# Performance work log

Hardware: AMD Instinct MI355X
Metric: run time of the kernel (lower is better)

The kernel has to match this reference:

```python
import jax, jax.numpy as jnp
import numpy as np

B, L, D = 2, 1024, 512          # batch, seq_len, d_model
H, DK, DV, P = 8, 64, 64, 4     # heads, d_k, d_v, num masks
TEMP = DK ** 0.5
EPS = 1e-6


def setup_inputs() -> dict:
    key = jax.random.key(0)
    ks = jax.random.split(key, 11)
    s = 0.04  # ~xavier scale for these fan sizes
    q = jax.random.normal(ks[0], (B, L, D), jnp.float32)
    k = jax.random.normal(ks[1], (B, L, D), jnp.float32)
    v = jax.random.normal(ks[2], (B, L, D), jnp.float32)
    mask = (jax.random.uniform(ks[3], (P, 1, 1, L, L)) > 0.2).astype(jnp.float32)
    w_q = jax.random.normal(ks[4], (H * DK, D), jnp.float32) * s
    w_k = jax.random.normal(ks[5], (H * DK, D), jnp.float32) * s
    w_v = jax.random.normal(ks[6], (H * DV, D), jnp.float32) * s
    fc_w = jax.random.normal(ks[7], (D, H * DV), jnp.float32) * s
    fc_b = jnp.zeros((D,), jnp.float32)
    ln_g = jnp.ones((D,), jnp.float32)
    ln_b = jnp.zeros((D,), jnp.float32)
    return {"q": q, "k": k, "v": v, "mask": mask, "w_q": w_q, "w_k": w_k,
            "w_v": w_v, "fc_w": fc_w, "fc_b": fc_b, "ln_g": ln_g, "ln_b": ln_b}


def reference(q, k, v, mask, w_q, w_k, w_v, fc_w, fc_b, ln_g, ln_b):
    b, lq = q.shape[0], q.shape[1]
    lk = k.shape[1]
    residual = q
    # pre-LayerNorm on q (normalize_before=True)
    mu = jnp.mean(q, axis=-1, keepdims=True)
    var = jnp.mean(jnp.square(q - mu), axis=-1, keepdims=True)
    qn = (q - mu) * jax.lax.rsqrt(var + EPS) * ln_g + ln_b
    # projections -> [B,H,L,dk/dv]
    qh = jnp.einsum('bld,ed->ble', qn, w_q).reshape(b, lq, H, DK).transpose(0, 2, 1, 3)
    kh = jnp.einsum('bld,ed->ble', k, w_k).reshape(b, lk, H, DK).transpose(0, 2, 1, 3)
    vh = jnp.einsum('bld,ed->ble', v, w_v).reshape(b, lk, H, DV).transpose(0, 2, 1, 3)
    # shared scores, computed once: [B,H,Lq,Lk]
    attn = jnp.einsum('bhqd,bhkd->bhqk', qh / TEMP, kh)
    # per-mask additive bias, vectorized over P (dropout is identity in eval)
    ext = (1.0 - mask) * -10000.0                      # [P,1,1,Lq,Lk]
    probs = jax.nn.softmax(attn[None] + ext, axis=-1)  # [P,B,H,Lq,Lk]
    out = jnp.einsum('pbhqk,bhkd->pbhqd', probs, vh)   # [P,B,H,Lq,DV]
    out = out.transpose(0, 1, 3, 2, 4).reshape(P, b, lq, H * DV)
    out = jnp.einsum('pble,de->pbld', out, fc_w) + fc_b
    out = out + residual[None]
    return (out, attn)
```

## Files before the change

kernel.cpp:

```cpp
#include <hip/hip_runtime.h>
#include <math.h>

namespace {

constexpr int B = 2, L = 1024, D = 512, H = 8, DK = 64, DV = 64, P = 4;
constexpr float EPS = 1e-6f;
constexpr float ESHIFT = 16.0f;

typedef float f32x4 __attribute__((ext_vector_type(4)));
typedef short s16x8 __attribute__((ext_vector_type(8)));

__device__ inline unsigned short f2bf(float x) {
  union { float f; unsigned u; } v; v.f = x;
  unsigned r = v.u + 0x7fffu + ((v.u >> 16) & 1u);
  return (unsigned short)(r >> 16);
}

struct Cvt7 {
  const float* s[7];
  unsigned short* d[7];
  int cum[8];
};

__global__ __launch_bounds__(256) void prep_kernel(
    const float* __restrict__ x, const float* __restrict__ g,
    const float* __restrict__ bta, unsigned short* __restrict__ y, Cvt7 a) {
  int bid = blockIdx.x, t = threadIdx.x;
  if (bid < B * L) {
    const float* xr = x + (size_t)bid * D;
    unsigned short* yr = y + (size_t)bid * D;
    float v0 = xr[t], v1 = xr[t + 256];
    float s = v0 + v1;
#pragma unroll
    for (int off = 32; off; off >>= 1) s += __shfl_down(s, off, 64);
    __shared__ float red[4];
    if ((t & 63) == 0) red[t >> 6] = s;
    __syncthreads();
    float mu = (red[0] + red[1] + red[2] + red[3]) * (1.0f / D);
    float d0 = v0 - mu, d1 = v1 - mu;
    float vs = d0 * d0 + d1 * d1;
#pragma unroll
    for (int off = 32; off; off >>= 1) vs += __shfl_down(vs, off, 64);
    __syncthreads();
    if ((t & 63) == 0) red[t >> 6] = vs;
    __syncthreads();
    float var = (red[0] + red[1] + red[2] + red[3]) * (1.0f / D);
    float rstd = rsqrtf(var + EPS);
    yr[t] = f2bf(d0 * rstd * g[t] + bta[t]);
    yr[t + 256] = f2bf(d1 * rstd * g[t + 256] + bta[t + 256]);
  } else {
    int e4 = ((bid - B * L) * 256 + t) * 4;
    int ti = 0;
    while (e4 >= a.cum[ti + 1]) ++ti;
    int off = e4 - a.cum[ti];
    float4 v = *(const float4*)(a.s[ti] + off);
    ushort4 o;
    if (ti == 6) {
      o.x = v.x != 0.0f ? 0xFFFFu : 0u;
      o.y = v.y != 0.0f ? 0xFFFFu : 0u;
      o.z = v.z != 0.0f ? 0xFFFFu : 0u;
      o.w = v.w != 0.0f ? 0xFFFFu : 0u;
    } else {
      o.x = f2bf(v.x); o.y = f2bf(v.y); o.z = f2bf(v.z); o.w = f2bf(v.w);
    }
    *(ushort4*)(a.d[ti] + off) = o;
  }
}

template <bool BF16OUT>
__global__ __launch_bounds__(256) void bgemm_nt(
    const unsigned short* __restrict__ A, int lda, long sA0, long sA1,
    const unsigned short* __restrict__ Bm, int ldb, long sB0, long sB1,
    void* __restrict__ Cv, int ldc, long sC0, long sC1,
    int Z0, int K, float alpha,
    const float* __restrict__ bias, const float* __restrict__ resid, int rm) {
  int z = blockIdx.z;
  int z0 = z % Z0, z1 = z / Z0;
  A += (size_t)z0 * sA0 + (size_t)z1 * sA1;
  Bm += (size_t)z0 * sB0 + (size_t)z1 * sB1;
  size_t cOff = (size_t)z0 * sC0 + (size_t)z1 * sC1;
  int m0 = blockIdx.y * 128, n0 = blockIdx.x * 128;
  int t = threadIdx.x;
  int w = t >> 6, lane = t & 63, q4 = lane >> 4, ln16 = lane & 15;
  int wm = (w >> 1) * 64, wn = (w & 1) * 64;
  __shared__ __align__(16) unsigned short As[2][128][40];
  __shared__ __align__(16) unsigned short Bs[2][128][40];
  f32x4 acc[4][4];
#pragma unroll
  for (int i = 0; i < 4; ++i)
#pragma unroll
    for (int j = 0; j < 4; ++j)
#pragma unroll
      for (int r = 0; r < 4; ++r) acc[i][j][r] = 0.0f;
  int c0 = t, c1 = t + 256;
  const unsigned short* Ar0 = A + (size_t)(m0 + (c0 >> 2)) * lda + (c0 & 3) * 8;
  const unsigned short* Ar1 = A + (size_t)(m0 + (c1 >> 2)) * lda + (c1 & 3) * 8;
  const unsigned short* Br0 = Bm + (size_t)(n0 + (c0 >> 2)) * ldb + (c0 & 3) * 8;
  const unsigned short* Br1 = Bm + (size_t)(n0 + (c1 >> 2)) * ldb + (c1 & 3) * 8;
  {
    float4 a0 = *(const float4*)Ar0;
    float4 a1 = *(const float4*)Ar1;
    float4 b0 = *(const float4*)Br0;
    float4 b1 = *(const float4*)Br1;
    *(float4*)&As[0][c0 >> 2][(c0 & 3) * 8] = a0;
    *(float4*)&As[0][c1 >> 2][(c1 & 3) * 8] = a1;
    *(float4*)&Bs[0][c0 >> 2][(c0 & 3) * 8] = b0;
    *(float4*)&Bs[0][c1 >> 2][(c1 & 3) * 8] = b1;
  }
  int nIt = K >> 5;
  for (int it = 0; it < nIt; ++it) {
    int cur = it & 1;
    float4 na0, na1, nb0, nb1;
    if (it + 1 < nIt) {
      int kt = (it + 1) * 32;
      na0 = *(const float4*)(Ar0 + kt);
      na1 = *(const float4*)(Ar1 + kt);
      nb0 = *(const float4*)(Br0 + kt);
      nb1 = *(const float4*)(Br1 + kt);
    }
    __syncthreads();
    s16x8 af[4], bf[4];
#pragma unroll
    for (int mi = 0; mi < 4; ++mi)
      af[mi] = *(const s16x8*)&As[cur][wm + mi * 16 + ln16][q4 * 8];
#pragma unroll
    for (int ni = 0; ni < 4; ++ni)
      bf[ni] = *(const s16x8*)&Bs[cur][wn + ni * 16 + ln16][q4 * 8];
#pragma unroll
    for (int mi = 0; mi < 4; ++mi)
#pragma unroll
      for (int ni = 0; ni < 4; ++ni)
        acc[mi][ni] = __builtin_amdgcn_mfma_f32_16x16x32_bf16(
            af[mi], bf[ni], acc[mi][ni], 0, 0, 0);
    if (it + 1 < nIt) {
      int nb = 1 - cur;
      *(float4*)&As[nb][c0 >> 2][(c0 & 3) * 8] = na0;
      *(float4*)&As[nb][c1 >> 2][(c1 & 3) * 8] = na1;
      *(float4*)&Bs[nb][c0 >> 2][(c0 & 3) * 8] = nb0;
      *(float4*)&Bs[nb][c1 >> 2][(c1 & 3) * 8] = nb1;
    }
  }
#pragma unroll
  for (int mi = 0; mi < 4; ++mi)
#pragma unroll
    for (int r = 0; r < 4; ++r) {
      int row = m0 + wm + mi * 16 + q4 * 4 + r;
#pragma unroll
      for (int ni = 0; ni < 4; ++ni) {
        int col = n0 + wn + ni * 16 + ln16;
        float v = acc[mi][ni][r] * alpha;
        if (bias) v += bias[col];
        if (resid) v += resid[(size_t)(row & rm) * ldc + col];
        if (BF16OUT)
          ((unsigned short*)Cv)[cOff + (size_t)row * ldc + col] = f2bf(v);
        else
          ((float*)Cv)[cOff + (size_t)row * ldc + col] = v;
      }
    }
}

__global__ __launch_bounds__(256) void vtrans(
    const unsigned short* __restrict__ vh, unsigned short* __restrict__ vt) {
  int bh = blockIdx.y, l0 = blockIdx.x * 64;
  int b = bh >> 3, h = bh & 7;
  __shared__ __align__(16) unsigned short T[64][72];
  int t = threadIdx.x;
  int lr = t >> 2, k16 = (t & 3) * 16;
  const unsigned short* src =
      vh + (size_t)(b * L + l0 + lr) * 512 + h * 64 + k16;
  float4 x0 = *(const float4*)src;
  float4 x1 = *(const float4*)(src + 8);
  *(float4*)&T[lr][k16] = x0;
  *(float4*)&T[lr][k16 + 8] = x1;
  __syncthreads();
  int dv = t >> 2, l16 = (t & 3) * 16;
  union { unsigned short u[16]; float4 f[2]; } o;
#pragma unroll
  for (int j = 0; j < 16; ++j) o.u[j] = T[l16 + j][dv];
  unsigned short* dst = vt + (size_t)(bh * 64 + dv) * 1024 + l0 + l16;
  *(float4*)dst = o.f[0];
  *(float4*)(dst + 8) = o.f[1];
}

__global__ __launch_bounds__(512) void fattn_kernel(
    const unsigned short* __restrict__ qh, const unsigned short* __restrict__ khm,
    const unsigned short* __restrict__ mb, const unsigned short* __restrict__ vt,
    float* __restrict__ attn, unsigned short* __restrict__ outh) {
  int q0 = blockIdx.x * 64, bh = blockIdx.y;
  int b = bh >> 3, h = bh & 7;
  __shared__ __align__(16) unsigned short EMs[2][4][64][72];
  __shared__ __align__(16) unsigned short Vs[2][64][72];
  __shared__ __align__(16) unsigned short Es[2][64][72];
  __shared__ __align__(16) unsigned short Qs[64][72];
  int t = threadIdx.x;
  int w = t >> 6, lane = t & 63, q4 = lane >> 4, ln16 = lane & 15;
  int p = w & 3, kh32 = (w >> 2) * 32;
  int qw = w & 3, nlo = (w >> 2) * 2;
  int er = t >> 3, ek = (t & 7) * 8;
  const unsigned short* mrow = mb + (size_t)(q0 + er) * L + ek;
  const unsigned short* vsrc = vt + ((size_t)bh * 64 + er) * L + ek;
  const unsigned short* kbase = khm + (size_t)(b * L) * 512 + h * 64;
  float* arow = attn + (size_t)bh * L * L + (size_t)q0 * L;

  s16x8 ones;
#pragma unroll
  for (int j = 0; j < 8; ++j) ones[j] = (short)0x3F80;
  f32x4 acc[4][4], accs[4];
#pragma unroll
  for (int i = 0; i < 4; ++i) {
#pragma unroll
    for (int r = 0; r < 4; ++r) accs[i][r] = 0.0f;
#pragma unroll
    for (int j = 0; j < 4; ++j)
#pragma unroll
      for (int r = 0; r < 4; ++r) acc[i][j][r] = 0.0f;
  }
  s16x8 kreg[2][2];
  int4 m4[4], v4;

#define KLOAD(dd)                                                              \
  do {                                                                         \
    int kc_ = (dd) * 64;                                                       \
    const unsigned short* kb_ =                                                \
        kbase + (size_t)(kc_ + nlo * 16 + ln16) * 512 + q4 * 8;                \
    kreg[0][0] = *(const s16x8*)kb_;                                           \
    kreg[0][1] = *(const s16x8*)(kb_ + 32);                                    \
    kreg[1][0] = *(const s16x8*)(kb_ + 16 * 512);                              \
    kreg[1][1] = *(const s16x8*)(kb_ + 16 * 512 + 32);                         \
  } while (0)

#define QKCHUNK(dd)                                                            \
  do {                                                                         \
    f32x4 a2[4][2];                                                            \
    _Pragma("unroll") for (int mi = 0; mi < 4; ++mi)                           \
        _Pragma("unroll") for (int j = 0; j < 2; ++j)                          \
            _Pragma("unroll") for (int r = 0; r < 4; ++r) a2[mi][j][r] = 0.0f; \
    _Pragma("unroll") for (int kk = 0; kk < 2; ++kk)                           \
        _Pragma("unroll") for (int mi = 0; mi < 4; ++mi) {                     \
      s16x8 qf = *(const s16x8*)&Qs[mi * 16 + ln16][kk * 32 + q4 * 8];         \
      a2[mi][0] = __builtin_amdgcn_mfma_f32_16x16x32_bf16(qf, kreg[0][kk],     \
                                                          a2[mi][0], 0, 0, 0); \
      a2[mi][1] = __builtin_amdgcn_mfma_f32_16x16x32_bf16(qf, kreg[1][kk],     \
                                                          a2[mi][1], 0, 0, 0); \
    }                                                                          \
    int kc_ = (dd) * 64, eb_ = (dd) & 1;                                       \
    _Pragma("unroll") for (int mi = 0; mi < 4; ++mi)                           \
        _Pragma("unroll") for (int r = 0; r < 4; ++r) {                        \
      int row_ = mi * 16 + q4 * 4 + r;                                         \
      _Pragma("unroll") for (int j = 0; j < 2; ++j) {                          \
        int col_ = (nlo + j) * 16 + ln16;                                      \
        float v_ = a2[mi][j][r] * 0.125f;                                      \
        arow[(size_t)row_ * L + kc_ + col_] = v_;                              \
        Es[eb_][row_][col_] = f2bf(__expf(v_ - ESHIFT));                       \
      }                                                                        \
    }                                                                          \
  } while (0)

  {
    const unsigned short* qrow =
        qh + (size_t)(b * L + q0 + er) * 512 + h * 64 + ek;
    *(int4*)&Qs[er][ek] = *(const int4*)qrow;
  }
#pragma unroll
  for (int pp = 0; pp < 4; ++pp)
    m4[pp] = *(const int4*)(mrow + (size_t)pp * L * L);
  v4 = *(const int4*)vsrc;
  KLOAD(qw);
  __syncthreads();
  if (qw == 0) QKCHUNK(0);
  else if (qw == 1) QKCHUNK(1);
  __syncthreads();
  {
    int4 e4 = *(const int4*)&Es[0][er][ek];
#pragma unroll
    for (int pp = 0; pp < 4; ++pp) {
      int4 em;
      em.x = e4.x & m4[pp].x; em.y = e4.y & m4[pp].y;
      em.z = e4.z & m4[pp].z; em.w = e4.w & m4[pp].w;
      *(int4*)&EMs[0][pp][er][ek] = em;
    }
    *(int4*)&Vs[0][er][ek] = v4;
  }
  __syncthreads();

  for (int c = 0; c < 16; ++c) {
    int buf = c & 1;
    if (c < 15) {
      int kc = (c + 1) * 64;
#pragma unroll
      for (int pp = 0; pp < 4; ++pp)
        m4[pp] = *(const int4*)(mrow + (size_t)pp * L * L + kc);
      v4 = *(const int4*)(vsrc + kc);
    }
    if (c + 4 <= 15 && ((c + 4) & 3) == qw) KLOAD(c + 4);
    s16x8 af[4], bfv[4];
#pragma unroll
    for (int mi = 0; mi < 4; ++mi)
      af[mi] = *(const s16x8*)&EMs[buf][p][mi * 16 + ln16][kh32 + q4 * 8];
#pragma unroll
    for (int ni = 0; ni < 4; ++ni)
      bfv[ni] = *(const s16x8*)&Vs[buf][ni * 16 + ln16][kh32 + q4 * 8];
#pragma unroll
    for (int mi = 0; mi < 4; ++mi) {
#pragma unroll
      for (int ni = 0; ni < 4; ++ni)
        acc[mi][ni] = __builtin_amdgcn_mfma_f32_16x16x32_bf16(
            af[mi], bfv[ni], acc[mi][ni], 0, 0, 0);
      accs[mi] = __builtin_amdgcn_mfma_f32_16x16x32_bf16(af[mi], ones,
                                                         accs[mi], 0, 0, 0);
    }
    if (c + 2 <= 15 && ((c + 2) & 3) == qw) QKCHUNK(c + 2);
    if (c < 15) {
      int nb = buf ^ 1;
      int4 e4 = *(const int4*)&Es[nb][er][ek];
#pragma unroll
      for (int pp = 0; pp < 4; ++pp) {
        int4 em;
        em.x = e4.x & m4[pp].x; em.y = e4.y & m4[pp].y;
        em.z = e4.z & m4[pp].z; em.w = e4.w & m4[pp].w;
        *(int4*)&EMs[nb][pp][er][ek] = em;
      }
      *(int4*)&Vs[nb][er][ek] = v4;
    }
    __syncthreads();
  }
#undef KLOAD
#undef QKCHUNK

  float* sc1 = (float*)&EMs[0][0][0][0];
  float* sc2 = (float*)&Vs[0][0][0];
  int wl = (w & 3) * 64 + lane;
  if (w >= 4) {
#pragma unroll
    for (int mi = 0; mi < 4; ++mi) {
#pragma unroll
      for (int ni = 0; ni < 4; ++ni)
#pragma unroll
        for (int r = 0; r < 4; ++r)
          sc1[((mi * 4 + ni) * 4 + r) * 257 + wl] = acc[mi][ni][r];
#pragma unroll
      for (int r = 0; r < 4; ++r)
        sc2[(mi * 4 + r) * 257 + wl] = accs[mi][r];
    }
  }
  __syncthreads();
  if (w < 4) {
#pragma unroll
    for (int mi = 0; mi < 4; ++mi) {
#pragma unroll
      for (int ni = 0; ni < 4; ++ni)
#pragma unroll
        for (int r = 0; r < 4; ++r)
          acc[mi][ni][r] += sc1[((mi * 4 + ni) * 4 + r) * 257 + wl];
#pragma unroll
      for (int r = 0; r < 4; ++r)
        accs[mi][r] += sc2[(mi * 4 + r) * 257 + wl];
    }
#pragma unroll
    for (int mi = 0; mi < 4; ++mi)
#pragma unroll
      for (int r = 0; r < 4; ++r) {
        int row = mi * 16 + q4 * 4 + r;
        float inv = 1.0f / accs[mi][r];
        size_t o = ((size_t)(p * B + b) * L + q0 + row) * 512 + h * 64 + ln16;
#pragma unroll
        for (int ni = 0; ni < 4; ++ni)
          outh[o + ni * 16] = f2bf(acc[mi][ni][r] * inv);
      }
  }
}

}

extern "C" void kernel_launch(void* const* d_in, const int* in_sizes, int n_in,
                              void* d_out, int out_size, void* d_ws,
                              size_t ws_size, hipStream_t stream) {
  const float* q = (const float*)d_in[0];
  const float* k = (const float*)d_in[1];
  const float* v = (const float*)d_in[2];
  const float* mask = (const float*)d_in[3];
  const float* w_q = (const float*)d_in[4];
  const float* w_k = (const float*)d_in[5];
  const float* w_v = (const float*)d_in[6];
  const float* fc_w = (const float*)d_in[7];
  const float* fc_b = (const float*)d_in[8];
  const float* ln_g = (const float*)d_in[9];
  const float* ln_b = (const float*)d_in[10];

  float* out = (float*)d_out;
  float* attn = out + (size_t)P * B * L * D;

  unsigned short* wsu = (unsigned short*)d_ws;
  const size_t T1 = (size_t)B * L * D;
  const size_t TW = (size_t)D * D;
  unsigned short* qkv_bf = wsu;
  unsigned short* w_bf = qkv_bf + 3 * T1;
  unsigned short* fcw_bf = w_bf + 3 * TW;
  unsigned short* qh_bf = fcw_bf + TW;
  unsigned short* vt = qh_bf + 3 * T1;
  unsigned short* outh = vt + T1;
  unsigned short* mask_us = outh + 4 * T1;

  Cvt7 ca;
  ca.s[0] = k; ca.s[1] = v; ca.s[2] = w_q; ca.s[3] = w_k; ca.s[4] = w_v;
  ca.s[5] = fc_w; ca.s[6] = mask;
  ca.d[0] = qkv_bf + T1; ca.d[1] = qkv_bf + 2 * T1;
  ca.d[2] = w_bf; ca.d[3] = w_bf + TW; ca.d[4] = w_bf + 2 * TW;
  ca.d[5] = fcw_bf; ca.d[6] = mask_us;
  ca.cum[0] = 0;
  int sizes[7] = {(int)T1, (int)T1, (int)TW, (int)TW, (int)TW, (int)TW,
                  P * L * L};
  for (int i = 0; i < 7; ++i) ca.cum[i + 1] = ca.cum[i] + sizes[i];
  prep_kernel<<<B * L + ca.cum[7] / 1024, 256, 0, stream>>>(q, ln_g, ln_b,
                                                            qkv_bf, ca);

  bgemm_nt<true><<<dim3(D / 128, (B * L) / 128, 3), 256, 0, stream>>>(
      qkv_bf, D, (long)T1, 0, w_bf, D, (long)TW, 0, qh_bf, D, (long)T1, 0,
      3, D, 1.0f, nullptr, nullptr, 0);

  vtrans<<<dim3(L / 64, B * H), 256, 0, stream>>>(qh_bf + 2 * T1, vt);

  fattn_kernel<<<dim3(L / 64, B * H), 512, 0, stream>>>(
      qh_bf, qh_bf + T1, mask_us, vt, attn, outh);

  bgemm_nt<false><<<dim3(D / 128, (P * B * L) / 128, 1), 256, 0, stream>>>(
      outh, D, 0, 0, fcw_bf, D, 0, 0, out, D, 0, 0, 1, D, 1.0f, fc_b, q,
      B * L - 1);
}
```

Before: 205.6 us.

## Bit-pack masks, fuse V transpose into projection GEMM, retile attention kernel

The mask is packed to one bit per element in the prep kernel, replacing the 16-bit mask buffer, and the attention kernel expands those bits into register masks on the exp tile, so the masked-E tiles per mask no longer go through shared memory. The V projection GEMM writes its output directly in transposed layout, which removes the separate vtrans kernel. The attention kernel moves to 32-query tiles with 256 threads, where each wave handles one mask p over the full K, dropping the cross-wave reduction through shared memory. The costs are extra bit-manipulation ALU work, scattered ushort4 transposed stores, and twice as many blocks that each recompute QK and exp.

```diff
diff --git a/kernel.cpp b/kernel.cpp
--- a/kernel.cpp
+++ b/kernel.cpp
@@ -16,17 +16,21 @@
   return (unsigned short)(r >> 16);
 }
 
-struct Cvt7 {
-  const float* s[7];
-  unsigned short* d[7];
-  int cum[8];
+struct Cvt6 {
+  const float* s[6];
+  unsigned short* d[6];
+  int cum[7];
 };
+constexpr int LNB = B * L;
+constexpr int CVB = 3072;
+constexpr int MKB = 512;
 
 __global__ __launch_bounds__(256) void prep_kernel(
     const float* __restrict__ x, const float* __restrict__ g,
-    const float* __restrict__ bta, unsigned short* __restrict__ y, Cvt7 a) {
+    const float* __restrict__ bta, unsigned short* __restrict__ y, Cvt6 a,
+    const float* __restrict__ mask, unsigned* __restrict__ mpk) {
   int bid = blockIdx.x, t = threadIdx.x;
-  if (bid < B * L) {
+  if (bid < LNB) {
     const float* xr = x + (size_t)bid * D;
     unsigned short* yr = y + (size_t)bid * D;
     float v0 = xr[t], v1 = xr[t + 256];
@@ -48,32 +52,39 @@
     float rstd = rsqrtf(var + EPS);
     yr[t] = f2bf(d0 * rstd * g[t] + bta[t]);
     yr[t + 256] = f2bf(d1 * rstd * g[t + 256] + bta[t + 256]);
-  } else {
-    int e4 = ((bid - B * L) * 256 + t) * 4;
+  } else if (bid < LNB + CVB) {
+    int e4 = ((bid - LNB) * 256 + t) * 4;
     int ti = 0;
     while (e4 >= a.cum[ti + 1]) ++ti;
     int off = e4 - a.cum[ti];
     float4 v = *(const float4*)(a.s[ti] + off);
     ushort4 o;
-    if (ti == 6) {
-      o.x = v.x != 0.0f ? 0xFFFFu : 0u;
-      o.y = v.y != 0.0f ? 0xFFFFu : 0u;
-      o.z = v.z != 0.0f ? 0xFFFFu : 0u;
-      o.w = v.w != 0.0f ? 0xFFFFu : 0u;
-    } else {
-      o.x = f2bf(v.x); o.y = f2bf(v.y); o.z = f2bf(v.z); o.w = f2bf(v.w);
-    }
+    o.x = f2bf(v.x); o.y = f2bf(v.y); o.z = f2bf(v.z); o.w = f2bf(v.w);
     *(ushort4*)(a.d[ti] + off) = o;
-  }
-}
-
-template <bool BF16OUT>
+  } else {
+    int gid = (bid - LNB - CVB) * 256 + t;
+    const float4* src = (const float4*)mask + (size_t)gid * 8;
+    unsigned bits = 0;
+#pragma unroll
+    for (int j = 0; j < 8; ++j) {
+      float4 vv = src[j];
+      bits |= (vv.x != 0.0f ? 1u : 0u) << (j * 4);
+      bits |= (vv.y != 0.0f ? 2u : 0u) << (j * 4);
+      bits |= (vv.z != 0.0f ? 4u : 0u) << (j * 4);
+      bits |= (vv.w != 0.0f ? 8u : 0u) << (j * 4);
+    }
+    mpk[gid] = bits;
+  }
+}
+
+template <bool BF16OUT, bool VTOUT>
 __global__ __launch_bounds__(256) void bgemm_nt(
     const unsigned short* __restrict__ A, int lda, long sA0, long sA1,
     const unsigned short* __restrict__ Bm, int ldb, long sB0, long sB1,
     void* __restrict__ Cv, int ldc, long sC0, long sC1,
     int Z0, int K, float alpha,
-    const float* __restrict__ bias, const float* __restrict__ resid, int rm) {
+    const float* __restrict__ bias, const float* __restrict__ resid, int rm,
+    unsigned short* __restrict__ vtout) {
   int z = blockIdx.z;
   int z0 = z % Z0, z1 = z / Z0;
   A += (size_t)z0 * sA0 + (size_t)z1 * sA1;
@@ -140,6 +151,24 @@
       *(float4*)&Bs[nb][c1 >> 2][(c1 & 3) * 8] = nb1;
     }
   }
+  if (VTOUT && z0 == 2) {
+#pragma unroll
+    for (int mi = 0; mi < 4; ++mi)
+#pragma unroll
+      for (int ni = 0; ni < 4; ++ni) {
+        int row0 = m0 + wm + mi * 16 + q4 * 4;
+        int col = n0 + wn + ni * 16 + ln16;
+        int bb = row0 >> 10, hh = col >> 6, dv = col & 63;
+        ushort4 o;
+        o.x = f2bf(acc[mi][ni][0]);
+        o.y = f2bf(acc[mi][ni][1]);
+        o.z = f2bf(acc[mi][ni][2]);
+        o.w = f2bf(acc[mi][ni][3]);
+        *(ushort4*)&vtout[((size_t)((bb * 8 + hh) * 64 + dv)) * 1024 +
+                          (row0 & 1023)] = o;
+      }
+    return;
+  }
 #pragma unroll
   for (int mi = 0; mi < 4; ++mi)
 #pragma unroll
@@ -159,55 +188,32 @@
     }
 }
 
-__global__ __launch_bounds__(256) void vtrans(
-    const unsigned short* __restrict__ vh, unsigned short* __restrict__ vt) {
-  int bh = blockIdx.y, l0 = blockIdx.x * 64;
+__global__ __launch_bounds__(256, 2) void fattn2_kernel(
+    const unsigned short* __restrict__ qh,
+    const unsigned short* __restrict__ khm, const unsigned* __restrict__ mpk,
+    const unsigned short* __restrict__ vt, float* __restrict__ attn,
+    unsigned short* __restrict__ outh) {
+  int q0 = blockIdx.x * 32, bh = blockIdx.y;
   int b = bh >> 3, h = bh & 7;
-  __shared__ __align__(16) unsigned short T[64][72];
-  int t = threadIdx.x;
-  int lr = t >> 2, k16 = (t & 3) * 16;
-  const unsigned short* src =
-      vh + (size_t)(b * L + l0 + lr) * 512 + h * 64 + k16;
-  float4 x0 = *(const float4*)src;
-  float4 x1 = *(const float4*)(src + 8);
-  *(float4*)&T[lr][k16] = x0;
-  *(float4*)&T[lr][k16 + 8] = x1;
-  __syncthreads();
-  int dv = t >> 2, l16 = (t & 3) * 16;
-  union { unsigned short u[16]; float4 f[2]; } o;
-#pragma unroll
-  for (int j = 0; j < 16; ++j) o.u[j] = T[l16 + j][dv];
-  unsigned short* dst = vt + (size_t)(bh * 64 + dv) * 1024 + l0 + l16;
-  *(float4*)dst = o.f[0];
-  *(float4*)(dst + 8) = o.f[1];
-}
-
-__global__ __launch_bounds__(512) void fattn_kernel(
-    const unsigned short* __restrict__ qh, const unsigned short* __restrict__ khm,
-    const unsigned short* __restrict__ mb, const unsigned short* __restrict__ vt,
-    float* __restrict__ attn, unsigned short* __restrict__ outh) {
-  int q0 = blockIdx.x * 64, bh = blockIdx.y;
-  int b = bh >> 3, h = bh & 7;
-  __shared__ __align__(16) unsigned short EMs[2][4][64][72];
+  __shared__ __align__(16) unsigned short Es[3][32][72];
   __shared__ __align__(16) unsigned short Vs[2][64][72];
-  __shared__ __align__(16) unsigned short Es[2][64][72];
-  __shared__ __align__(16) unsigned short Qs[64][72];
+  __shared__ __align__(16) unsigned short Qs[32][72];
+  __shared__ unsigned Mb[2][4][32][2];
   int t = threadIdx.x;
   int w = t >> 6, lane = t & 63, q4 = lane >> 4, ln16 = lane & 15;
-  int p = w & 3, kh32 = (w >> 2) * 32;
-  int qw = w & 3, nlo = (w >> 2) * 2;
-  int er = t >> 3, ek = (t & 7) * 8;
-  const unsigned short* mrow = mb + (size_t)(q0 + er) * L + ek;
-  const unsigned short* vsrc = vt + ((size_t)bh * 64 + er) * L + ek;
+  int vr = t >> 2, vk = (t & 3) * 16;
+  int mp = t >> 6, mq = (t >> 1) & 31, md = t & 1;
+  const unsigned short* vsrc = vt + ((size_t)bh * 64 + vr) * 1024 + vk;
+  const unsigned* msrc = mpk + ((size_t)mp * L + q0 + mq) * 32 + md;
   const unsigned short* kbase = khm + (size_t)(b * L) * 512 + h * 64;
   float* arow = attn + (size_t)bh * L * L + (size_t)q0 * L;
 
   s16x8 ones;
 #pragma unroll
   for (int j = 0; j < 8; ++j) ones[j] = (short)0x3F80;
-  f32x4 acc[4][4], accs[4];
-#pragma unroll
-  for (int i = 0; i < 4; ++i) {
+  f32x4 acc[2][4], accs[2];
+#pragma unroll
+  for (int i = 0; i < 2; ++i) {
 #pragma unroll
     for (int r = 0; r < 4; ++r) accs[i][r] = 0.0f;
 #pragma unroll
@@ -215,41 +221,40 @@
 #pragma unroll
       for (int r = 0; r < 4; ++r) acc[i][j][r] = 0.0f;
   }
-  s16x8 kreg[2][2];
-  int4 m4[4], v4;
+  s16x8 kreg[4][2];
 
 #define KLOAD(dd)                                                              \
   do {                                                                         \
-    int kc_ = (dd) * 64;                                                       \
     const unsigned short* kb_ =                                                \
-        kbase + (size_t)(kc_ + nlo * 16 + ln16) * 512 + q4 * 8;                \
-    kreg[0][0] = *(const s16x8*)kb_;                                           \
-    kreg[0][1] = *(const s16x8*)(kb_ + 32);                                    \
-    kreg[1][0] = *(const s16x8*)(kb_ + 16 * 512);                              \
-    kreg[1][1] = *(const s16x8*)(kb_ + 16 * 512 + 32);                         \
+        kbase + (size_t)((dd) * 64 + ln16) * 512 + q4 * 8;                     \
+    _Pragma("unroll") for (int ni = 0; ni < 4; ++ni)                           \
+        _Pragma("unroll") for (int kk = 0; kk < 2; ++kk)                       \
+            kreg[ni][kk] = *(const s16x8*)(kb_ + (size_t)ni * 16 * 512 +       \
+                                           kk * 32);                           \
   } while (0)
 
 #define QKCHUNK(dd)                                                            \
   do {                                                                         \
-    f32x4 a2[4][2];                                                            \
-    _Pragma("unroll") for (int mi = 0; mi < 4; ++mi)                           \
-        _Pragma("unroll") for (int j = 0; j < 2; ++j)                          \
-            _Pragma("unroll") for (int r = 0; r < 4; ++r) a2[mi][j][r] = 0.0f; \
-    _Pragma("unroll") for (int kk = 0; kk < 2; ++kk)                           \
-        _Pragma("unroll") for (int mi = 0; mi < 4; ++mi) {                     \
-      s16x8 qf = *(const s16x8*)&Qs[mi * 16 + ln16][kk * 32 + q4 * 8];         \
-      a2[mi][0] = __builtin_amdgcn_mfma_f32_16x16x32_bf16(qf, kreg[0][kk],     \
-                                                          a2[mi][0], 0, 0, 0); \
-      a2[mi][1] = __builtin_amdgcn_mfma_f32_16x16x32_bf16(qf, kreg[1][kk],     \
-                                                          a2[mi][1], 0, 0, 0); \
+    f32x4 a2[2][4];                                                            \
+    _Pragma("unroll") for (int mi = 0; mi < 2; ++mi)                           \
+        _Pragma("unroll") for (int ni = 0; ni < 4; ++ni)                       \
+            _Pragma("unroll") for (int r = 0; r < 4; ++r) a2[mi][ni][r] = 0.f; \
+    _Pragma("unroll") for (int kk = 0; kk < 2; ++kk) {                         \
+      s16x8 qf[2];                                                             \
+      _Pragma("unroll") for (int mi = 0; mi < 2; ++mi) qf[mi] =                \
+          *(const s16x8*)&Qs[mi * 16 + ln16][kk * 32 + q4 * 8];                \
+      _Pragma("unroll") for (int mi = 0; mi < 2; ++mi)                         \
+          _Pragma("unroll") for (int ni = 0; ni < 4; ++ni)                     \
+              a2[mi][ni] = __builtin_amdgcn_mfma_f32_16x16x32_bf16(            \
+                  qf[mi], kreg[ni][kk], a2[mi][ni], 0, 0, 0);                  \
     }                                                                          \
-    int kc_ = (dd) * 64, eb_ = (dd) & 1;                                       \
-    _Pragma("unroll") for (int mi = 0; mi < 4; ++mi)                           \
+    int kc_ = (dd) * 64, eb_ = (dd) % 3;                                       \
+    _Pragma("unroll") for (int mi = 0; mi < 2; ++mi)                           \
         _Pragma("unroll") for (int r = 0; r < 4; ++r) {                        \
       int row_ = mi * 16 + q4 * 4 + r;                                         \
-      _Pragma("unroll") for (int j = 0; j < 2; ++j) {                          \
-        int col_ = (nlo + j) * 16 + ln16;                                      \
-        float v_ = a2[mi][j][r] * 0.125f;                                      \
+      _Pragma("unroll") for (int ni = 0; ni < 4; ++ni) {                       \
+        int col_ = ni * 16 + ln16;                                             \
+        float v_ = a2[mi][ni][r] * 0.125f;                                     \
         arow[(size_t)row_ * L + kc_ + col_] = v_;                              \
         Es[eb_][row_][col_] = f2bf(__expf(v_ - ESHIFT));                       \
       }                                                                        \
@@ -257,117 +262,90 @@
   } while (0)
 
   {
-    const unsigned short* qrow =
-        qh + (size_t)(b * L + q0 + er) * 512 + h * 64 + ek;
-    *(int4*)&Qs[er][ek] = *(const int4*)qrow;
-  }
-#pragma unroll
-  for (int pp = 0; pp < 4; ++pp)
-    m4[pp] = *(const int4*)(mrow + (size_t)pp * L * L);
-  v4 = *(const int4*)vsrc;
-  KLOAD(qw);
+    int qr = t >> 3, qk = (t & 7) * 8;
+    *(int4*)&Qs[qr][qk] =
+        *(const int4*)(qh + (size_t)(b * L + q0 + qr) * 512 + h * 64 + qk);
+  }
+  *(int4*)&Vs[0][vr][vk] = *(const int4*)vsrc;
+  *(int4*)&Vs[0][vr][vk + 8] = *(const int4*)(vsrc + 8);
+  Mb[0][mp][mq][md] = msrc[0];
+  KLOAD(w);
   __syncthreads();
-  if (qw == 0) QKCHUNK(0);
-  else if (qw == 1) QKCHUNK(1);
+  if (w == 0) QKCHUNK(0);
+  else if (w == 1) QKCHUNK(1);
   __syncthreads();
-  {
-    int4 e4 = *(const int4*)&Es[0][er][ek];
-#pragma unroll
-    for (int pp = 0; pp < 4; ++pp) {
-      int4 em;
-      em.x = e4.x & m4[pp].x; em.y = e4.y & m4[pp].y;
-      em.z = e4.z & m4[pp].z; em.w = e4.w & m4[pp].w;
-      *(int4*)&EMs[0][pp][er][ek] = em;
-    }
-    *(int4*)&Vs[0][er][ek] = v4;
-  }
-  __syncthreads();
 
   for (int c = 0; c < 16; ++c) {
-    int buf = c & 1;
+    int4 nv0, nv1;
+    unsigned nmb;
     if (c < 15) {
-      int kc = (c + 1) * 64;
-#pragma unroll
-      for (int pp = 0; pp < 4; ++pp)
-        m4[pp] = *(const int4*)(mrow + (size_t)pp * L * L + kc);
-      v4 = *(const int4*)(vsrc + kc);
-    }
-    if (c + 4 <= 15 && ((c + 4) & 3) == qw) KLOAD(c + 4);
-    s16x8 af[4], bfv[4];
-#pragma unroll
-    for (int mi = 0; mi < 4; ++mi)
-      af[mi] = *(const s16x8*)&EMs[buf][p][mi * 16 + ln16][kh32 + q4 * 8];
-#pragma unroll
-    for (int ni = 0; ni < 4; ++ni)
-      bfv[ni] = *(const s16x8*)&Vs[buf][ni * 16 + ln16][kh32 + q4 * 8];
-#pragma unroll
-    for (int mi = 0; mi < 4; ++mi) {
+      const unsigned short* vs = vsrc + (c + 1) * 64;
+      nv0 = *(const int4*)vs;
+      nv1 = *(const int4*)(vs + 8);
+      nmb = msrc[(c + 1) * 2];
+    }
+    if (c + 4 <= 15 && ((c + 4) & 3) == w) KLOAD(c + 4);
+    {
+      int b3 = c % 3, bv = c & 1;
+      unsigned mby[2][2];
+#pragma unroll
+      for (int mi = 0; mi < 2; ++mi) {
+        unsigned d0 = Mb[bv][w][mi * 16 + ln16][0];
+        unsigned d1 = Mb[bv][w][mi * 16 + ln16][1];
+        mby[mi][0] = (d0 >> (q4 * 8)) & 0xFFu;
+        mby[mi][1] = (d1 >> (q4 * 8)) & 0xFFu;
+      }
+      s16x8 bfv[4][2];
 #pragma unroll
       for (int ni = 0; ni < 4; ++ni)
-        acc[mi][ni] = __builtin_amdgcn_mfma_f32_16x16x32_bf16(
-            af[mi], bfv[ni], acc[mi][ni], 0, 0, 0);
-      accs[mi] = __builtin_amdgcn_mfma_f32_16x16x32_bf16(af[mi], ones,
-                                                         accs[mi], 0, 0, 0);
-    }
-    if (c + 2 <= 15 && ((c + 2) & 3) == qw) QKCHUNK(c + 2);
+#pragma unroll
+        for (int kk = 0; kk < 2; ++kk)
+          bfv[ni][kk] =
+              *(const s16x8*)&Vs[bv][ni * 16 + ln16][kk * 32 + q4 * 8];
+#pragma unroll
+      for (int mi = 0; mi < 2; ++mi)
+#pragma unroll
+        for (int kk = 0; kk < 2; ++kk) {
+          union { s16x8 s; unsigned u[4]; } ef;
+          ef.s = *(const s16x8*)&Es[b3][mi * 16 + ln16][kk * 32 + q4 * 8];
+          unsigned bb = mby[mi][kk];
+#pragma unroll
+          for (int dd = 0; dd < 4; ++dd) {
+            unsigned mm = (((bb >> (2 * dd)) & 1u) ? 0xFFFFu : 0u) |
+                          (((bb >> (2 * dd + 1)) & 1u) ? 0xFFFF0000u : 0u);
+            ef.u[dd] &= mm;
+          }
+#pragma unroll
+          for (int ni = 0; ni < 4; ++ni)
+            acc[mi][ni] = __builtin_amdgcn_mfma_f32_16x16x32_bf16(
+                ef.s, bfv[ni][kk], acc[mi][ni], 0, 0, 0);
+          accs[mi] = __builtin_amdgcn_mfma_f32_16x16x32_bf16(ef.s, ones,
+                                                             accs[mi], 0, 0, 0);
+        }
+    }
+    if (c + 2 <= 15 && ((c + 2) & 3) == w) QKCHUNK(c + 2);
     if (c < 15) {
-      int nb = buf ^ 1;
-      int4 e4 = *(const int4*)&Es[nb][er][ek];
-#pragma unroll
-      for (int pp = 0; pp < 4; ++pp) {
-        int4 em;
-        em.x = e4.x & m4[pp].x; em.y = e4.y & m4[pp].y;
-        em.z = e4.z & m4[pp].z; em.w = e4.w & m4[pp].w;
-        *(int4*)&EMs[nb][pp][er][ek] = em;
-      }
-      *(int4*)&Vs[nb][er][ek] = v4;
+      int nb = (c + 1) & 1;
+      *(int4*)&Vs[nb][vr][vk] = nv0;
+      *(int4*)&Vs[nb][vr][vk + 8] = nv1;
+      Mb[nb][mp][mq][md] = nmb;
     }
     __syncthreads();
   }
 #undef KLOAD
 #undef QKCHUNK
 
-  float* sc1 = (float*)&EMs[0][0][0][0];
-  float* sc2 = (float*)&Vs[0][0][0];
-  int wl = (w & 3) * 64 + lane;
-  if (w >= 4) {
-#pragma unroll
-    for (int mi = 0; mi < 4; ++mi) {
+#pragma unroll
+  for (int mi = 0; mi < 2; ++mi)
+#pragma unroll
+    for (int r = 0; r < 4; ++r) {
+      int row = mi * 16 + q4 * 4 + r;
+      float inv = 1.0f / accs[mi][r];
+      size_t o = ((size_t)(w * B + b) * L + q0 + row) * 512 + h * 64 + ln16;
 #pragma unroll
       for (int ni = 0; ni < 4; ++ni)
-#pragma unroll
-        for (int r = 0; r < 4; ++r)
-          sc1[((mi * 4 + ni) * 4 + r) * 257 + wl] = acc[mi][ni][r];
-#pragma unroll
-      for (int r = 0; r < 4; ++r)
-        sc2[(mi * 4 + r) * 257 + wl] = accs[mi][r];
-    }
-  }
-  __syncthreads();
-  if (w < 4) {
-#pragma unroll
-    for (int mi = 0; mi < 4; ++mi) {
-#pragma unroll
-      for (int ni = 0; ni < 4; ++ni)
-#pragma unroll
-        for (int r = 0; r < 4; ++r)
-          acc[mi][ni][r] += sc1[((mi * 4 + ni) * 4 + r) * 257 + wl];
-#pragma unroll
-      for (int r = 0; r < 4; ++r)
-        accs[mi][r] += sc2[(mi * 4 + r) * 257 + wl];
-    }
-#pragma unroll
-    for (int mi = 0; mi < 4; ++mi)
-#pragma unroll
-      for (int r = 0; r < 4; ++r) {
-        int row = mi * 16 + q4 * 4 + r;
-        float inv = 1.0f / accs[mi][r];
-        size_t o = ((size_t)(p * B + b) * L + q0 + row) * 512 + h * 64 + ln16;
-#pragma unroll
-        for (int ni = 0; ni < 4; ++ni)
-          outh[o + ni * 16] = f2bf(acc[mi][ni][r] * inv);
-      }
-  }
+        outh[o + ni * 16] = f2bf(acc[mi][ni][r] * inv);
+    }
 }
 
 }
@@ -397,33 +375,31 @@
   unsigned short* w_bf = qkv_bf + 3 * T1;
   unsigned short* fcw_bf = w_bf + 3 * TW;
   unsigned short* qh_bf = fcw_bf + TW;
-  unsigned short* vt = qh_bf + 3 * T1;
+  unsigned short* vt = qh_bf + 2 * T1;
   unsigned short* outh = vt + T1;
-  unsigned short* mask_us = outh + 4 * T1;
-
-  Cvt7 ca;
+  unsigned* mpk = (unsigned*)(outh + 4 * T1);
+
+  Cvt6 ca;
   ca.s[0] = k; ca.s[1] = v; ca.s[2] = w_q; ca.s[3] = w_k; ca.s[4] = w_v;
-  ca.s[5] = fc_w; ca.s[6] = mask;
+  ca.s[5] = fc_w;
   ca.d[0] = qkv_bf + T1; ca.d[1] = qkv_bf + 2 * T1;
   ca.d[2] = w_bf; ca.d[3] = w_bf + TW; ca.d[4] = w_bf + 2 * TW;
-  ca.d[5] = fcw_bf; ca.d[6] = mask_us;
+  ca.d[5] = fcw_bf;
   ca.cum[0] = 0;
-  int sizes[7] = {(int)T1, (int)T1, (int)TW, (int)TW, (int)TW, (int)TW,
-                  P * L * L};
-  for (int i = 0; i < 7; ++i) ca.cum[i + 1] = ca.cum[i] + sizes[i];
-  prep_kernel<<<B * L + ca.cum[7] / 1024, 256, 0, stream>>>(q, ln_g, ln_b,
-                                                            qkv_bf, ca);
-
-  bgemm_nt<true><<<dim3(D / 128, (B * L) / 128, 3), 256, 0, stream>>>(
+  int sizes[6] = {(int)T1, (int)T1, (int)TW, (int)TW, (int)TW, (int)TW};
+  for (int i = 0; i < 6; ++i) ca.cum[i + 1] = ca.cum[i] + sizes[i];
+  prep_kernel<<<LNB + CVB + MKB, 256, 0, stream>>>(q, ln_g, ln_b, qkv_bf, ca,
+                                                   mask, mpk);
+
+  bgemm_nt<true, true><<<dim3(D / 128, (B * L) / 128, 3), 256, 0, stream>>>(
       qkv_bf, D, (long)T1, 0, w_bf, D, (long)TW, 0, qh_bf, D, (long)T1, 0,
-      3, D, 1.0f, nullptr, nullptr, 0);
-
-  vtrans<<<dim3(L / 64, B * H), 256, 0, stream>>>(qh_bf + 2 * T1, vt);
-
-  fattn_kernel<<<dim3(L / 64, B * H), 512, 0, stream>>>(
-      qh_bf, qh_bf + T1, mask_us, vt, attn, outh);
-
-  bgemm_nt<false><<<dim3(D / 128, (P * B * L) / 128, 1), 256, 0, stream>>>(
+      3, D, 1.0f, nullptr, nullptr, 0, vt);
+
+  fattn2_kernel<<<dim3(L / 32, B * H), 256, 0, stream>>>(
+      qh_bf, qh_bf + T1, mpk, vt, attn, outh);
+
+  bgemm_nt<false, false><<<dim3(D / 128, (P * B * L) / 128, 1), 256, 0,
+                           stream>>>(
       outh, D, 0, 0, fcw_bf, D, 0, 0, out, D, 0, 0, 1, D, 1.0f, fc_b, q,
-      B * L - 1);
-}
+      B * L - 1, nullptr);
+}
```

Result: faster. 198.8 us (-3.3%).
